# Performance work log

Measured on AMD Instinct MI355X. Metric: run time of the kernel, lower is better.

The kernel has to match this reference:

```python
import jax, jax.numpy as jnp
import numpy as np

P = 3
N_DIGITS = 4
MAX_IDX = 63  # module clamps indices with min(idx, 63)
EPS = 1e-10


def _padic_table(p=P, n_digits=N_DIGITS):
    n = p ** n_digits  # 81
    d = np.abs(np.arange(n)[:, None] - np.arange(n)[None, :])
    val = np.zeros((n, n), dtype=np.int64)
    tmp = d.copy()
    # valuation: count factors of p (at most ~n_digits*log levels; 8 iters is plenty for n=81)
    for _ in range(8):
        div = (tmp > 0) & (tmp % p == 0)
        val += div
        tmp = np.where(div, tmp // p, tmp)
    dist = np.where(d > 0, float(p) ** (-val.astype(np.float64)), 0.0)
    return jnp.asarray(dist, dtype=jnp.float32)


def setup_inputs() -> dict:
    key = jax.random.key(0)
    k1, k2 = jax.random.split(key)
    codon_embeddings = jax.random.normal(k1, (8, 1024, 256), dtype=jnp.float32)
    codon_indices = jax.random.randint(k2, (8, 1024), 0, 64)
    padic_distances = _padic_table()
    return {
        "codon_embeddings": codon_embeddings,
        "codon_indices": codon_indices,
        "padic_distances": padic_distances,
    }


def reference(codon_embeddings, codon_indices, padic_distances):
    B, S, D = codon_embeddings.shape
    x = codon_embeddings.reshape(-1, D)  # (N, D), N = B*S

    # Euclidean cdist (p=2): d2 = |xi|^2 + |xj|^2 - 2 xi.xj
    sq = jnp.sum(x * x, axis=-1)
    d2 = sq[:, None] + sq[None, :] - 2.0 * (x @ x.T)
    d2 = jnp.maximum(d2, 0.0)
    # safe sqrt (zero diag -> zero distance, no nan grads)
    emb_dist = jnp.where(d2 > 0, jnp.sqrt(jnp.where(d2 > 0, d2, 1.0)), 0.0)

    # vectorized equivalent of the python double-loop gather
    idx = jnp.minimum(codon_indices.reshape(-1), MAX_IDX)  # (N,)
    target_dist = padic_distances[idx][:, idx]  # (N, N)

    emb_n = emb_dist / (jnp.max(emb_dist) + EPS)
    tgt_n = target_dist / (jnp.max(target_dist) + EPS)

    e = emb_n.reshape(-1) - jnp.mean(emb_n)
    t = tgt_n.reshape(-1) - jnp.mean(tgt_n)
    corr = jnp.sum(e * t) / (jnp.sqrt(jnp.sum(e * e) * jnp.sum(t * t)) + EPS)
    return 1.0 - corr
```

## Files before the change

### kernel.cpp

```cpp
#include <hip/hip_runtime.h>
#include <math.h>

typedef __attribute__((ext_vector_type(8))) short short8;
typedef __attribute__((ext_vector_type(16))) float f32x16;

#if defined(__has_builtin)
#if __has_builtin(__builtin_amdgcn_global_load_lds)
#define HAVE_GLL 1
#endif
#if __has_builtin(__builtin_amdgcn_sqrtf)
#define FSQRT(x) __builtin_amdgcn_sqrtf(x)
#endif
#if __has_builtin(__builtin_amdgcn_cvt_pk_fp8_f32) && __has_builtin(__builtin_amdgcn_cvt_f32_fp8)
#define HAVE_CVT8 1
#endif
#endif
#ifndef HAVE_GLL
#define HAVE_GLL 0
#endif
#ifndef FSQRT
#define FSQRT(x) sqrtf(x)
#endif
#ifndef HAVE_CVT8
#define HAVE_CVT8 0
#endif

__device__ __forceinline__ unsigned short f2bf(float f) {
    unsigned int x = __float_as_uint(f);
    unsigned int r = (x + 0x7fffu + ((x >> 16) & 1u)) >> 16;
    return (unsigned short)r;
}

__device__ __forceinline__ unsigned char f2e4m3(float f) {
    unsigned u = __float_as_uint(f);
    unsigned s = (u >> 24) & 0x80u;
    float a = fabsf(f);
    if (a < 0.015625f) return (unsigned char)s;
    if (a > 448.f)     return (unsigned char)(s | 0x7E);
    unsigned au = u & 0x7FFFFFFFu;
    unsigned mlo = au & 0xFFFFFu;
    unsigned keep = au >> 20;
    keep += (mlo > 0x80000u) || (mlo == 0x80000u && (keep & 1u));
    int e = (int)(keep >> 3) - 127;
    unsigned m3 = keep & 7u;
    if (e < -6) return (unsigned char)s;
    if (e > 8)  return (unsigned char)(s | 0x7E);
    return (unsigned char)(s | (unsigned)((e + 7) << 3) | m3);
}
__device__ __forceinline__ float e4m3dec(unsigned char c) {
    if (!(c & 0x7F)) return 0.f;
    unsigned s = ((unsigned)(c & 0x80)) << 24;
    unsigned e = (c >> 3) & 0xF;
    unsigned m = c & 7u;
    return __uint_as_float(s | ((e - 7 + 127) << 23) | (m << 20));
}


__global__ void rowstats_kernel(const float* __restrict__ x, const int* __restrict__ idx,
                                float* __restrict__ sq, int* __restrict__ ci,
                                unsigned char* __restrict__ x8,
                                int N, int D, int doCvt) {
    int wave0 = (blockIdx.x * blockDim.x + threadIdx.x) >> 6;
    int lane  = threadIdx.x & 63;
    int nw    = (gridDim.x * blockDim.x) >> 6;
    for (int row = wave0; row < N; row += nw) {
        const float* rp = x + (size_t)row * D;
        float s = 0.f;
        for (int c = lane * 4; c < D; c += 256) {
            float4 v = *reinterpret_cast<const float4*>(rp + c);
            if (doCvt) {
#if HAVE_CVT8
                unsigned pk = 0;
                pk = (unsigned)__builtin_amdgcn_cvt_pk_fp8_f32(v.x, v.y, (int)pk, false);
                pk = (unsigned)__builtin_amdgcn_cvt_pk_fp8_f32(v.z, v.w, (int)pk, true);
                *reinterpret_cast<unsigned*>(x8 + (size_t)row * D + c) = pk;
                float q0 = __builtin_amdgcn_cvt_f32_fp8((int)pk, 0);
                float q1 = __builtin_amdgcn_cvt_f32_fp8((int)pk, 1);
                float q2 = __builtin_amdgcn_cvt_f32_fp8((int)pk, 2);
                float q3 = __builtin_amdgcn_cvt_f32_fp8((int)pk, 3);
#else
                uchar4 h;
                h.x = f2e4m3(v.x); h.y = f2e4m3(v.y); h.z = f2e4m3(v.z); h.w = f2e4m3(v.w);
                *reinterpret_cast<uchar4*>(x8 + (size_t)row * D + c) = h;
                float q0 = e4m3dec(h.x), q1 = e4m3dec(h.y), q2 = e4m3dec(h.z), q3 = e4m3dec(h.w);
#endif
                s = fmaf(q0, q0, s); s = fmaf(q1, q1, s);
                s = fmaf(q2, q2, s); s = fmaf(q3, q3, s);
            } else {
                s = fmaf(v.x, v.x, s); s = fmaf(v.y, v.y, s);
                s = fmaf(v.z, v.z, s); s = fmaf(v.w, v.w, s);
            }
        }
        #pragma unroll
        for (int o = 32; o > 0; o >>= 1) s += __shfl_down(s, o, 64);
        if (lane == 0) {
            sq[row] = s;
            int v = idx[row]; if (v > 63) v = 63;
            ci[row] = v;
        }
    }
}

__device__ __forceinline__ void tri_decode(int L, int NB, int chunks, int doSwz, int& bi, int& bj) {
    if (doSwz) { int xcd = L & 7, pos = L >> 3; L = xcd * chunks + pos; }
    float disc = (float)((2 * NB + 1) * (2 * NB + 1) - 8 * L);
    int b = (int)(((float)(2 * NB + 1) - sqrtf(disc)) * 0.5f);
    if (b < 0) b = 0; if (b > NB - 1) b = NB - 1;
    while (b + 1 <= NB - 1 && ((b + 1) * NB - ((b + 1) * b) / 2) <= L) ++b;
    while (b > 0 && (b * NB - (b * (b - 1)) / 2) > L) --b;
    bi = b; bj = b + (L - (b * NB - (b * (b - 1)) / 2));
}

template<bool DIAG>
__device__ __forceinline__ void epilogueQ(const f32x16 (&acc)[2][2],
                                          const float* sqA, const float* sqB,
                                          const int* caA, const int* cbB, const float* tbl,
                                          float* red, int w, int lane, int wr, int wc,
                                          double* partials, int pidx) {
    const int l31 = lane & 31;
    const int hi4 = (lane >> 5) << 2;
    float sb[2]; int cb[2];
    #pragma unroll
    for (int ni = 0; ni < 2; ++ni) {
        int c = wc * 64 + ni * 32 + l31;
        sb[ni] = sqB[c]; cb[ni] = cbB[c];
    }
    float se = 0.f, sd2 = 0.f, setv = 0.f;
    #pragma unroll
    for (int mi = 0; mi < 2; ++mi)
        #pragma unroll
        for (int r = 0; r < 16; ++r) {
            int rr = wr * 64 + mi * 32 + (r & 3) + ((r >> 2) << 3) + hi4;
            float sa_ = sqA[rr]; int ca_ = caA[rr];
            #pragma unroll
            for (int ni = 0; ni < 2; ++ni) {
                float d2 = fmaf(-2.f, acc[mi][ni][r], sa_ + sb[ni]);
                d2 = fmaxf(d2, 0.f);
                if (DIAG) { if (rr == wc * 64 + ni * 32 + l31) d2 = 0.f; }
                float e = FSQRT(d2);
                int delta = ca_ - cb[ni]; if (delta < 0) delta = -delta;
                float t = tbl[delta];
                se += e; sd2 += d2; setv = fmaf(e, t, setv);
            }
        }
    #pragma unroll
    for (int o = 32; o > 0; o >>= 1) {
        se  += __shfl_down(se, o, 64);
        sd2 += __shfl_down(sd2, o, 64);
        setv += __shfl_down(setv, o, 64);
    }
    if (lane == 0) { red[w * 3 + 0] = se; red[w * 3 + 1] = sd2; red[w * 3 + 2] = setv; }
    __syncthreads();
    if (w == 0 && lane == 0) {
        double wgt = DIAG ? 1.0 : 2.0;
        double S0 = 0, S1 = 0, S2 = 0;
        #pragma unroll
        for (int i = 0; i < 4; ++i) {
            S0 += (double)red[i * 3 + 0]; S1 += (double)red[i * 3 + 1]; S2 += (double)red[i * 3 + 2];
        }
        double* p = partials + (size_t)pidx * 4;
        p[0] = wgt * S0; p[1] = wgt * S1; p[2] = wgt * S2;
    }
}

__global__ __launch_bounds__(256, 4) void pair128f8_kernel(
        const unsigned char* __restrict__ x8, const float* __restrict__ table,
        const float* __restrict__ sq, const int* __restrict__ ci,
        int NB, int chunks, int doSwz, double* __restrict__ partials) {
#if HAVE_GLL
    constexpr int D = 256;
    __shared__ char lds[16384];
    __shared__ float sqA[128], sqB[128], tbl[64];
    __shared__ int   caA[128], cbB[128];
    __shared__ float red[12];

    int bi, bj;
    tri_decode(blockIdx.x, NB, chunks, doSwz, bi, bj);

    const int tid = threadIdx.x;
    const int w = tid >> 6, lane = tid & 63;
    const int wr = w >> 1, wc = w & 1;
    const int l31 = lane & 31, khalf = lane >> 5;

    if (tid < 64) tbl[tid] = table[tid];
    if (tid < 128) { sqA[tid] = sq[bi * 128 + tid]; caA[tid] = ci[bi * 128 + tid]; }
    else { int t2 = tid - 128; sqB[t2] = sq[bj * 128 + t2]; cbB[t2] = ci[bj * 128 + t2]; }

    const int pa_ = lane >> 3;
    const int pt  = ((lane & 7) - pa_) & 7;
    const int srow = pa_ * 4 + (pt >> 1);
    const int sh   = pt & 1;

    const int prow0 = ((w >= 2) ? bj : bi) * 128;
    auto STAGE4 = [&](int t) {
        #pragma unroll
        for (int q = 0; q < 4; ++q) {
            int u   = (w << 2) + q;
            int blk = (u >> 1) & 3;
            int kh  = u & 1;
            const unsigned char* g = x8 + (size_t)(prow0 + blk * 32 + srow) * D
                                        + t * 64 + kh * 32 + sh * 16;
            char* dst = lds + (u << 10);
            __builtin_amdgcn_global_load_lds(
                (__attribute__((address_space(1))) void*)(void*)g,
                (__attribute__((address_space(3))) void*)dst, 16, 0, 0);
        }
    };

    const int ra = l31 >> 2, rb = l31 & 3;
    const int pos0 = ra * 8 + ((2 * rb + 0 + ra) & 7);
    const int pos1 = ra * 8 + ((2 * rb + 1 + ra) & 7);

    f32x16 acc[2][2];
    #pragma unroll
    for (int a = 0; a < 2; ++a)
        #pragma unroll
        for (int b = 0; b < 2; ++b)
            #pragma unroll
            for (int r = 0; r < 16; ++r) acc[a][b][r] = 0.f;

    for (int t = 0; t < 4; ++t) {
        STAGE4(t);
        asm volatile("s_waitcnt vmcnt(0)" ::: "memory");
        __builtin_amdgcn_s_barrier();
        #pragma unroll
        for (int kh = 0; kh < 2; ++kh) {
            #pragma unroll
            for (int s = 0; s < 2; ++s) {
                const int fo = (s ? pos1 : pos0) * 16 + khalf * 8;
                long a_[2], b_[2];
                #pragma unroll
                for (int mi = 0; mi < 2; ++mi)
                    a_[mi] = *reinterpret_cast<const long*>(lds + (((((wr << 1) + mi) << 1) + kh) << 10) + fo);
                #pragma unroll
                for (int ni = 0; ni < 2; ++ni)
                    b_[ni] = *reinterpret_cast<const long*>(lds + ((8 + (((wc << 1) + ni) << 1) + kh) << 10) + fo);
                #pragma unroll
                for (int mi = 0; mi < 2; ++mi)
                    #pragma unroll
                    for (int ni = 0; ni < 2; ++ni)
                        acc[mi][ni] = __builtin_amdgcn_mfma_f32_32x32x16_fp8_fp8(a_[mi], b_[ni], acc[mi][ni], 0, 0, 0);
            }
        }
        __builtin_amdgcn_s_barrier();
    }

    if (bi == bj) epilogueQ<true >(acc, sqA, sqB, caA, cbB, tbl, red, w, lane, wr, wc, partials, blockIdx.x);
    else          epilogueQ<false>(acc, sqA, sqB, caA, cbB, tbl, red, w, lane, wr, wc, partials, blockIdx.x);
#endif
}

__global__ void pair_fb_kernel(const float* __restrict__ x, const float* __restrict__ table,
                               const float* __restrict__ sq, const int* __restrict__ ci,
                               int D, int NB, int chunks, int doSwz,
                               double* __restrict__ partials) {
    typedef __attribute__((ext_vector_type(4))) float f32x4v;
    int bi, bj;
    tri_decode(blockIdx.x, NB, chunks, doSwz, bi, bj);

    __shared__ float sqA[128], sqB[128], tbl[64];
    __shared__ int   caA[128], cbB[128];
    __shared__ float red[12];

    const int tid = threadIdx.x;
    const int w = tid >> 6, lane = tid & 63;
    const int wr = w >> 1, wc = w & 1;
    const int l15 = lane & 15, koct = lane >> 4;

    if (tid < 64) tbl[tid] = table[tid];
    if (tid < 128) { sqA[tid] = sq[bi * 128 + tid]; caA[tid] = ci[bi * 128 + tid]; }
    else { int t2 = tid - 128; sqB[t2] = sq[bj * 128 + t2]; cbB[t2] = ci[bj * 128 + t2]; }
    __syncthreads();

    f32x4v acc[4][4];
    #pragma unroll
    for (int a = 0; a < 4; ++a)
        #pragma unroll
        for (int b = 0; b < 4; ++b) acc[a][b] = (f32x4v){0.f, 0.f, 0.f, 0.f};

    const float* pa = x + (size_t)(bi * 128 + wr * 64 + l15) * D + koct * 8;
    const float* pb = x + (size_t)(bj * 128 + wc * 64 + l15) * D + koct * 8;
    const size_t rs = (size_t)16 * D;
    for (int k = 0; k < D; k += 32) {
        short8 af[4], bfv[4];
        #pragma unroll
        for (int m = 0; m < 4; ++m) {
            float4 f0 = *reinterpret_cast<const float4*>(pa + m * rs + k);
            float4 f1 = *reinterpret_cast<const float4*>(pa + m * rs + k + 4);
            short8 v;
            v[0]=(short)f2bf(f0.x); v[1]=(short)f2bf(f0.y); v[2]=(short)f2bf(f0.z); v[3]=(short)f2bf(f0.w);
            v[4]=(short)f2bf(f1.x); v[5]=(short)f2bf(f1.y); v[6]=(short)f2bf(f1.z); v[7]=(short)f2bf(f1.w);
            af[m] = v;
        }
        #pragma unroll
        for (int n = 0; n < 4; ++n) {
            float4 f0 = *reinterpret_cast<const float4*>(pb + n * rs + k);
            float4 f1 = *reinterpret_cast<const float4*>(pb + n * rs + k + 4);
            short8 v;
            v[0]=(short)f2bf(f0.x); v[1]=(short)f2bf(f0.y); v[2]=(short)f2bf(f0.z); v[3]=(short)f2bf(f0.w);
            v[4]=(short)f2bf(f1.x); v[5]=(short)f2bf(f1.y); v[6]=(short)f2bf(f1.z); v[7]=(short)f2bf(f1.w);
            bfv[n] = v;
        }
        #pragma unroll
        for (int fm = 0; fm < 4; ++fm)
            #pragma unroll
            for (int fn = 0; fn < 4; ++fn)
                acc[fm][fn] = __builtin_amdgcn_mfma_f32_16x16x32_bf16(af[fm], bfv[fn], acc[fm][fn], 0, 0, 0);
    }

    const int rsub = koct << 2;
    float sb[4]; int cb[4];
    #pragma unroll
    for (int fn = 0; fn < 4; ++fn) {
        int c = wc * 64 + fn * 16 + l15;
        sb[fn] = sqB[c]; cb[fn] = cbB[c];
    }
    float se = 0.f, sd2 = 0.f, setv = 0.f;
    const bool diag = (bi == bj);
    #pragma unroll
    for (int fm = 0; fm < 4; ++fm)
        #pragma unroll
        for (int rg = 0; rg < 4; ++rg) {
            int r = wr * 64 + fm * 16 + rsub + rg;
            float sa_ = sqA[r]; int ca_ = caA[r];
            #pragma unroll
            for (int fn = 0; fn < 4; ++fn) {
                float d2 = fmaf(-2.f, acc[fm][fn][rg], sa_ + sb[fn]);
                d2 = fmaxf(d2, 0.f);
                if (diag && r == wc * 64 + fn * 16 + l15) d2 = 0.f;
                float e = FSQRT(d2);
                int delta = ca_ - cb[fn]; if (delta < 0) delta = -delta;
                float t = tbl[delta];
                se += e; sd2 += d2; setv = fmaf(e, t, setv);
            }
        }
    #pragma unroll
    for (int o = 32; o > 0; o >>= 1) {
        se  += __shfl_down(se, o, 64);
        sd2 += __shfl_down(sd2, o, 64);
        setv += __shfl_down(setv, o, 64);
    }
    if (lane == 0) { red[w * 3 + 0] = se; red[w * 3 + 1] = sd2; red[w * 3 + 2] = setv; }
    __syncthreads();
    if (tid == 0) {
        double wgt = diag ? 1.0 : 2.0;
        double S0 = 0, S1 = 0, S2 = 0;
        #pragma unroll
        for (int i = 0; i < 4; ++i) {
            S0 += (double)red[i * 3 + 0]; S1 += (double)red[i * 3 + 1]; S2 += (double)red[i * 3 + 2];
        }
        double* p = partials + (size_t)blockIdx.x * 4;
        p[0] = wgt * S0; p[1] = wgt * S1; p[2] = wgt * S2;
    }
}

__global__ void finalize_kernel(const double* __restrict__ partials, int nL,
                                const int* __restrict__ civ, int N,
                                const float* __restrict__ table, int tdim,
                                float* __restrict__ out) {
    __shared__ unsigned int h[64];
    __shared__ double red[4][5];
    const int tid = threadIdx.x;
    if (tid < 64) h[tid] = 0u;
    __syncthreads();
    for (int i = tid; i < N; i += 256) atomicAdd(&h[civ[i]], 1u);
    __syncthreads();

    double se = 0, sd2 = 0, setv = 0;
    for (int i = tid; i < nL; i += 256) {
        const double* p = partials + (size_t)i * 4;
        se += p[0]; sd2 += p[1]; setv += p[2];
    }
    double st = 0, stt = 0;
    for (int c = tid; c < 4096; c += 256) {
        int u = c >> 6, v = c & 63;
        double t = (double)table[u * tdim + v];
        double hh = (double)h[u] * (double)h[v];
        st += hh * t; stt += hh * t * t;
    }
    #pragma unroll
    for (int o = 32; o > 0; o >>= 1) {
        se += __shfl_down(se, o, 64);
        sd2 += __shfl_down(sd2, o, 64);
        setv += __shfl_down(setv, o, 64);
        st += __shfl_down(st, o, 64);
        stt += __shfl_down(stt, o, 64);
    }
    int w = tid >> 6;
    if ((tid & 63) == 0) { red[w][0] = se; red[w][1] = sd2; red[w][2] = setv; red[w][3] = st; red[w][4] = stt; }
    __syncthreads();
    if (tid == 0) {
        double S[5] = {0, 0, 0, 0, 0};
        #pragma unroll
        for (int i = 0; i < 4; ++i)
            #pragma unroll
            for (int q = 0; q < 5; ++q) S[q] += red[i][q];
        double nn = (double)N * (double)N;
        double cet = S[2] - S[0] * S[3] / nn;
        double cee = S[1] - S[0] * S[0] / nn;
        double ctt = S[4] - S[3] * S[3] / nn;
        double corr = cet / (sqrt(cee * ctt) + 1e-10);
        out[0] = (float)(1.0 - corr);
    }
}

extern "C" void kernel_launch(void* const* d_in, const int* in_sizes, int n_in,
                              void* d_out, int out_size, void* d_ws, size_t ws_size,
                              hipStream_t stream) {
    const float* x     = (const float*)d_in[0];
    const int*   idx   = (const int*)d_in[1];
    const float* table = (const float*)d_in[2];

    const int N = in_sizes[1];
    const int D = in_sizes[0] / N;
    int tdim = 1;
    while (tdim * tdim < in_sizes[2]) ++tdim;

    char* ws = (char*)d_ws;
    double*        partials = (double*)(ws + 512);
    float*         sqv      = (float*)(ws + 67584);
    int*           civ      = (int*)(ws + 67584 + (size_t)N * 4);
    unsigned char* x8       = (unsigned char*)(ws + 67584 + (size_t)N * 8);

    size_t need = 67584 + (size_t)N * 8 + (size_t)N * D;
    const bool f8 = (ws_size >= need) && (D == 256) && (N % 128 == 0);

    rowstats_kernel<<<dim3(1024), 256, 0, stream>>>(x, idx, sqv, civ, x8, N, D, f8 ? 1 : 0);

    const int NB = N / 128;
    const int nL = NB * (NB + 1) / 2;
    const int doSwz = (nL % 8 == 0) ? 1 : 0;
    const int chunks = nL / 8;

    if (f8)
        pair128f8_kernel<<<dim3(nL), 256, 0, stream>>>(x8, table, sqv, civ, NB, chunks, doSwz, partials);
    else
        pair_fb_kernel<<<dim3(nL), 256, 0, stream>>>(x, table, sqv, civ, D, NB, chunks, doSwz, partials);

    finalize_kernel<<<1, 256, 0, stream>>>(partials, nL, civ, N, table, tdim, (float*)d_out);
}
```

Measured before the change: 45.47 us.

## Stage full K extent into LDS up front and drop per-step barriers

The fp8 pair kernel now issues all four K-slice global-to-LDS loads at once into a 64KB dynamic shared buffer, waits once, then runs every MFMA step with no further barriers. This removes the serialized load-wait-compute-barrier loop so memory latency is paid once per tile. In exchange LDS use per block grows to about 66KB, launch bounds drop to 2 blocks per SM, and a hipFuncSetAttribute call is added to each launch, which lowers occupancy and adds host overhead.

```diff
diff --git a/kernel.cpp b/kernel.cpp
--- a/kernel.cpp
+++ b/kernel.cpp
@@ -163,16 +163,27 @@
     }
 }
 
-__global__ __launch_bounds__(256, 4) void pair128f8_kernel(
+#define F8W_LDS_BYTES 67888
+#define F8W_TBL  65536
+#define F8W_SQA  65792
+#define F8W_SQB  66304
+#define F8W_CAA  66816
+#define F8W_CBB  67328
+#define F8W_RED  67840
+
+__global__ __launch_bounds__(256, 2) void pair128f8w_kernel(
         const unsigned char* __restrict__ x8, const float* __restrict__ table,
         const float* __restrict__ sq, const int* __restrict__ ci,
         int NB, int chunks, int doSwz, double* __restrict__ partials) {
 #if HAVE_GLL
     constexpr int D = 256;
-    __shared__ char lds[16384];
-    __shared__ float sqA[128], sqB[128], tbl[64];
-    __shared__ int   caA[128], cbB[128];
-    __shared__ float red[12];
+    extern __shared__ char dyn[];
+    float* tbl = (float*)(dyn + F8W_TBL);
+    float* sqA = (float*)(dyn + F8W_SQA);
+    float* sqB = (float*)(dyn + F8W_SQB);
+    int*   caA = (int*)(dyn + F8W_CAA);
+    int*   cbB = (int*)(dyn + F8W_CBB);
+    float* red = (float*)(dyn + F8W_RED);
 
     int bi, bj;
     tri_decode(blockIdx.x, NB, chunks, doSwz, bi, bj);
@@ -200,7 +211,7 @@
             int kh  = u & 1;
             const unsigned char* g = x8 + (size_t)(prow0 + blk * 32 + srow) * D
                                         + t * 64 + kh * 32 + sh * 16;
-            char* dst = lds + (u << 10);
+            char* dst = dyn + (((t << 4) + u) << 10);
             __builtin_amdgcn_global_load_lds(
                 (__attribute__((address_space(1))) void*)(void*)g,
                 (__attribute__((address_space(3))) void*)dst, 16, 0, 0);
@@ -219,10 +230,13 @@
             #pragma unroll
             for (int r = 0; r < 16; ++r) acc[a][b][r] = 0.f;
 
+    STAGE4(0); STAGE4(1); STAGE4(2); STAGE4(3);
+    asm volatile("s_waitcnt vmcnt(0) lgkmcnt(0)" ::: "memory");
+    __builtin_amdgcn_s_barrier();
+
+    #pragma unroll
     for (int t = 0; t < 4; ++t) {
-        STAGE4(t);
-        asm volatile("s_waitcnt vmcnt(0)" ::: "memory");
-        __builtin_amdgcn_s_barrier();
+        const int tb = t << 4;
         #pragma unroll
         for (int kh = 0; kh < 2; ++kh) {
             #pragma unroll
@@ -231,10 +245,10 @@
                 long a_[2], b_[2];
                 #pragma unroll
                 for (int mi = 0; mi < 2; ++mi)
-                    a_[mi] = *reinterpret_cast<const long*>(lds + (((((wr << 1) + mi) << 1) + kh) << 10) + fo);
+                    a_[mi] = *reinterpret_cast<const long*>(dyn + ((tb + (((wr << 1) + mi) << 1) + kh) << 10) + fo);
                 #pragma unroll
                 for (int ni = 0; ni < 2; ++ni)
-                    b_[ni] = *reinterpret_cast<const long*>(lds + ((8 + (((wc << 1) + ni) << 1) + kh) << 10) + fo);
+                    b_[ni] = *reinterpret_cast<const long*>(dyn + ((tb + 8 + (((wc << 1) + ni) << 1) + kh) << 10) + fo);
                 #pragma unroll
                 for (int mi = 0; mi < 2; ++mi)
                     #pragma unroll
@@ -242,7 +256,6 @@
                         acc[mi][ni] = __builtin_amdgcn_mfma_f32_32x32x16_fp8_fp8(a_[mi], b_[ni], acc[mi][ni], 0, 0, 0);
             }
         }
-        __builtin_amdgcn_s_barrier();
     }
 
     if (bi == bj) epilogueQ<true >(acc, sqA, sqB, caA, cbB, tbl, red, w, lane, wr, wc, partials, blockIdx.x);
@@ -423,7 +436,13 @@
     unsigned char* x8       = (unsigned char*)(ws + 67584 + (size_t)N * 8);
 
     size_t need = 67584 + (size_t)N * 8 + (size_t)N * D;
-    const bool f8 = (ws_size >= need) && (D == 256) && (N % 128 == 0);
+    bool f8 = (ws_size >= need) && (D == 256) && (N % 128 == 0);
+    if (f8) {
+        hipError_t e = hipFuncSetAttribute((const void*)pair128f8w_kernel,
+                                           hipFuncAttributeMaxDynamicSharedMemorySize,
+                                           F8W_LDS_BYTES);
+        f8 = (e == hipSuccess);
+    }
 
     rowstats_kernel<<<dim3(1024), 256, 0, stream>>>(x, idx, sqv, civ, x8, N, D, f8 ? 1 : 0);
 
@@ -433,7 +452,7 @@
     const int chunks = nL / 8;
 
     if (f8)
-        pair128f8_kernel<<<dim3(nL), 256, 0, stream>>>(x8, table, sqv, civ, NB, chunks, doSwz, partials);
+        pair128f8w_kernel<<<dim3(nL), 256, F8W_LDS_BYTES, stream>>>(x8, table, sqv, civ, NB, chunks, doSwz, partials);
     else
         pair_fb_kernel<<<dim3(nL), 256, 0, stream>>>(x, table, sqv, civ, D, NB, chunks, doSwz, partials);
 
```

Measured after the change: 53.19 us. 1.17x slower.

## Add 64x64 triangular-tile fp8 pair kernel to raise block count

Applied to the files above, without the earlier changes.

Adds a new pair kernel that processes 64x64 upper-triangular tiles with fp8 MFMA. Each of its four waves computes one 32x32 sub-tile, and operands are staged through a small 8KB LDS buffer via global_load_lds. The launcher now prefers this path, which launches 8256 blocks for N=8192 instead of 2080, to improve occupancy and load balance. The cost is more total operand reloads, more partial sums for finalize to reduce, and a per-k-step sync with no double buffering.

```diff
diff --git a/kernel.cpp b/kernel.cpp
--- a/kernel.cpp
+++ b/kernel.cpp
@@ -54,7 +54,6 @@
     unsigned m = c & 7u;
     return __uint_as_float(s | ((e - 7 + 127) << 23) | (m << 20));
 }
-
 
 __global__ void rowstats_kernel(const float* __restrict__ x, const int* __restrict__ idx,
                                 float* __restrict__ sq, int* __restrict__ ci,
@@ -111,6 +110,126 @@
     bi = b; bj = b + (L - (b * NB - (b * (b - 1)) / 2));
 }
 
+__global__ __launch_bounds__(256, 8) void pair64f8_kernel(
+        const unsigned char* __restrict__ x8, const float* __restrict__ table,
+        const float* __restrict__ sq, const int* __restrict__ ci,
+        int NB, int chunks, int doSwz, double* __restrict__ partials) {
+#if HAVE_GLL
+    constexpr int D = 256;
+    __shared__ char lds[8192];
+    __shared__ float sqA[64], sqB[64], tbl[64];
+    __shared__ int   caA[64], cbB[64];
+    __shared__ float red[12];
+
+    int bi, bj;
+    tri_decode(blockIdx.x, NB, chunks, doSwz, bi, bj);
+
+    const int tid = threadIdx.x;
+    const int w = tid >> 6, lane = tid & 63;
+    const int wr = w >> 1, wc = w & 1;
+    const int l31 = lane & 31, khalf = lane >> 5;
+
+    if (tid < 64) tbl[tid] = table[tid];
+    else if (tid < 128) { int r = tid - 64;  sqA[r] = sq[bi * 64 + r]; caA[r] = ci[bi * 64 + r]; }
+    else if (tid < 192) { int r = tid - 128; sqB[r] = sq[bj * 64 + r]; cbB[r] = ci[bj * 64 + r]; }
+
+    const int pa_ = lane >> 3;
+    const int pt  = ((lane & 7) - pa_) & 7;
+    const int srow = pa_ * 4 + (pt >> 1);
+    const int sh   = pt & 1;
+
+    const int u0 = w << 1;
+    const unsigned char* g0;
+    const unsigned char* g1;
+    {
+        int uA = u0, uB = u0 + 1;
+        int p0 = (uA < 4) ? (bi * 64 + (uA >> 1) * 32) : (bj * 64 + ((uA - 4) >> 1) * 32);
+        int p1 = (uB < 4) ? (bi * 64 + (uB >> 1) * 32) : (bj * 64 + ((uB - 4) >> 1) * 32);
+        g0 = x8 + (size_t)(p0 + srow) * D + (uA & 1) * 32 + sh * 16;
+        g1 = x8 + (size_t)(p1 + srow) * D + (uB & 1) * 32 + sh * 16;
+    }
+    char* dst0 = lds + (u0 << 10);
+    char* dst1 = lds + ((u0 + 1) << 10);
+
+    const int ra = l31 >> 2, rb = l31 & 3;
+    const int fo0 = (ra * 8 + ((2 * rb + 0 + ra) & 7)) * 16 + khalf * 8;
+    const int fo1 = (ra * 8 + ((2 * rb + 1 + ra) & 7)) * 16 + khalf * 8;
+
+    const char* a0b = lds + (((wr << 1) | 0) << 10);
+    const char* a1b = lds + (((wr << 1) | 1) << 10);
+    const char* b0b = lds + ((4 + (wc << 1) + 0) << 10);
+    const char* b1b = lds + ((4 + (wc << 1) + 1) << 10);
+
+    f32x16 acc;
+    #pragma unroll
+    for (int r = 0; r < 16; ++r) acc[r] = 0.f;
+
+    for (int t = 0; t < 4; ++t) {
+        __builtin_amdgcn_global_load_lds(
+            (__attribute__((address_space(1))) void*)(void*)g0,
+            (__attribute__((address_space(3))) void*)dst0, 16, 0, 0);
+        __builtin_amdgcn_global_load_lds(
+            (__attribute__((address_space(1))) void*)(void*)g1,
+            (__attribute__((address_space(3))) void*)dst1, 16, 0, 0);
+        g0 += 64; g1 += 64;
+        asm volatile("s_waitcnt vmcnt(0)" ::: "memory");
+        __builtin_amdgcn_s_barrier();
+        {
+            long aA, bB;
+            aA = *reinterpret_cast<const long*>(a0b + fo0);
+            bB = *reinterpret_cast<const long*>(b0b + fo0);
+            acc = __builtin_amdgcn_mfma_f32_32x32x16_fp8_fp8(aA, bB, acc, 0, 0, 0);
+            aA = *reinterpret_cast<const long*>(a0b + fo1);
+            bB = *reinterpret_cast<const long*>(b0b + fo1);
+            acc = __builtin_amdgcn_mfma_f32_32x32x16_fp8_fp8(aA, bB, acc, 0, 0, 0);
+            aA = *reinterpret_cast<const long*>(a1b + fo0);
+            bB = *reinterpret_cast<const long*>(b1b + fo0);
+            acc = __builtin_amdgcn_mfma_f32_32x32x16_fp8_fp8(aA, bB, acc, 0, 0, 0);
+            aA = *reinterpret_cast<const long*>(a1b + fo1);
+            bB = *reinterpret_cast<const long*>(b1b + fo1);
+            acc = __builtin_amdgcn_mfma_f32_32x32x16_fp8_fp8(aA, bB, acc, 0, 0, 0);
+        }
+        __builtin_amdgcn_s_barrier();
+    }
+
+    const int lcol = wc * 32 + l31;
+    const float sb = sqB[lcol];
+    const int   cb = cbB[lcol];
+    const int hi4 = khalf << 2;
+    float se = 0.f, sd2 = 0.f, setv = 0.f;
+    const bool diag = (bi == bj);
+    #pragma unroll
+    for (int r = 0; r < 16; ++r) {
+        int lrow = wr * 32 + (r & 3) + ((r >> 2) << 3) + hi4;
+        float d2 = fmaf(-2.f, acc[r], sqA[lrow] + sb);
+        d2 = fmaxf(d2, 0.f);
+        if (diag && lrow == lcol) d2 = 0.f;
+        float e = FSQRT(d2);
+        int delta = caA[lrow] - cb; if (delta < 0) delta = -delta;
+        float tt = tbl[delta];
+        se += e; sd2 += d2; setv = fmaf(e, tt, setv);
+    }
+    #pragma unroll
+    for (int o = 32; o > 0; o >>= 1) {
+        se  += __shfl_down(se, o, 64);
+        sd2 += __shfl_down(sd2, o, 64);
+        setv += __shfl_down(setv, o, 64);
+    }
+    if (lane == 0) { red[w * 3 + 0] = se; red[w * 3 + 1] = sd2; red[w * 3 + 2] = setv; }
+    __syncthreads();
+    if (tid == 0) {
+        double wgt = diag ? 1.0 : 2.0;
+        double S0 = 0, S1 = 0, S2 = 0;
+        #pragma unroll
+        for (int i = 0; i < 4; ++i) {
+            S0 += (double)red[i * 3 + 0]; S1 += (double)red[i * 3 + 1]; S2 += (double)red[i * 3 + 2];
+        }
+        double* p = partials + (size_t)blockIdx.x * 4;
+        p[0] = wgt * S0; p[1] = wgt * S1; p[2] = wgt * S2;
+    }
+#endif
+}
+
 template<bool DIAG>
 __device__ __forceinline__ void epilogueQ(const f32x16 (&acc)[2][2],
                                           const float* sqA, const float* sqB,
@@ -417,25 +536,41 @@
     while (tdim * tdim < in_sizes[2]) ++tdim;
 
     char* ws = (char*)d_ws;
-    double*        partials = (double*)(ws + 512);
-    float*         sqv      = (float*)(ws + 67584);
-    int*           civ      = (int*)(ws + 67584 + (size_t)N * 4);
-    unsigned char* x8       = (unsigned char*)(ws + 67584 + (size_t)N * 8);
-
-    size_t need = 67584 + (size_t)N * 8 + (size_t)N * D;
-    const bool f8 = (ws_size >= need) && (D == 256) && (N % 128 == 0);
-
-    rowstats_kernel<<<dim3(1024), 256, 0, stream>>>(x, idx, sqv, civ, x8, N, D, f8 ? 1 : 0);
-
-    const int NB = N / 128;
-    const int nL = NB * (NB + 1) / 2;
-    const int doSwz = (nL % 8 == 0) ? 1 : 0;
-    const int chunks = nL / 8;
-
-    if (f8)
-        pair128f8_kernel<<<dim3(nL), 256, 0, stream>>>(x8, table, sqv, civ, NB, chunks, doSwz, partials);
-    else
-        pair_fb_kernel<<<dim3(nL), 256, 0, stream>>>(x, table, sqv, civ, D, NB, chunks, doSwz, partials);
-
-    finalize_kernel<<<1, 256, 0, stream>>>(partials, nL, civ, N, table, tdim, (float*)d_out);
-}
+
+    const int NB64 = N / 64,  nL64  = NB64 * (NB64 + 1) / 2;
+    const int NB128 = N / 128, nL128 = NB128 * (NB128 + 1) / 2;
+    size_t part64_b = ((size_t)nL64 * 32 + 511) & ~(size_t)511;
+    size_t need64  = 512 + part64_b + (size_t)N * 8 + (size_t)N * D;
+    size_t need128 = 67584 + (size_t)N * 8 + (size_t)N * D;
+
+    const bool p64  = (ws_size >= need64)  && (D == 256) && (N % 64 == 0);
+    const bool p128 = !p64 && (ws_size >= need128) && (D == 256) && (N % 128 == 0);
+
+    if (p64) {
+        double*        partials = (double*)(ws + 512);
+        float*         sqv      = (float*)(ws + 512 + part64_b);
+        int*           civ      = (int*)(ws + 512 + part64_b + (size_t)N * 4);
+        unsigned char* x8       = (unsigned char*)(ws + 512 + part64_b + (size_t)N * 8);
+        rowstats_kernel<<<dim3(1024), 256, 0, stream>>>(x, idx, sqv, civ, x8, N, D, 1);
+        const int doSwz = (nL64 % 8 == 0) ? 1 : 0;
+        pair64f8_kernel<<<dim3(nL64), 256, 0, stream>>>(x8, table, sqv, civ, NB64, nL64 / 8, doSwz, partials);
+        finalize_kernel<<<1, 256, 0, stream>>>(partials, nL64, civ, N, table, tdim, (float*)d_out);
+    } else if (p128) {
+        double*        partials = (double*)(ws + 512);
+        float*         sqv      = (float*)(ws + 67584);
+        int*           civ      = (int*)(ws + 67584 + (size_t)N * 4);
+        unsigned char* x8       = (unsigned char*)(ws + 67584 + (size_t)N * 8);
+        rowstats_kernel<<<dim3(1024), 256, 0, stream>>>(x, idx, sqv, civ, x8, N, D, 1);
+        const int doSwz = (nL128 % 8 == 0) ? 1 : 0;
+        pair128f8_kernel<<<dim3(nL128), 256, 0, stream>>>(x8, table, sqv, civ, NB128, nL128 / 8, doSwz, partials);
+        finalize_kernel<<<1, 256, 0, stream>>>(partials, nL128, civ, N, table, tdim, (float*)d_out);
+    } else {
+        double* partials = (double*)(ws + 512);
+        float*  sqv      = (float*)(ws + 67584);
+        int*    civ      = (int*)(ws + 67584 + (size_t)N * 4);
+        rowstats_kernel<<<dim3(1024), 256, 0, stream>>>(x, idx, sqv, civ, (unsigned char*)0, N, D, 0);
+        const int doSwz = (nL128 % 8 == 0) ? 1 : 0;
+        pair_fb_kernel<<<dim3(nL128), 256, 0, stream>>>(x, table, sqv, civ, D, NB128, nL128 / 8, doSwz, partials);
+        finalize_kernel<<<1, 256, 0, stream>>>(partials, nL128, civ, N, table, tdim, (float*)d_out);
+    }
+}
```

Measured after the change: 59.46 us. 30.8% more time.

## Split each 128x128 pair tile across sixteen waves with one MFMA tile each

Applied to the files above, without the earlier changes.

The fp8 pair kernel now launches 1024 threads per block. Each of the 16 waves owns a single 32x32 accumulator tile instead of a 2x2 grid of tiles, and each wave stages exactly one 1KB LDS chunk per k-step. The epilogue is inlined and reduces across 16 waves. The aim is more waves in flight to hide LDS/global latency and shorten the per-wave MFMA and epilogue chain. The cost is that A/B fragments are no longer reused across tiles inside a wave, so LDS reads per MFMA double. The larger block also adds barrier cost and may reduce the number of resident blocks per CU.

```diff
diff --git a/kernel.cpp b/kernel.cpp
--- a/kernel.cpp
+++ b/kernel.cpp
@@ -54,7 +54,6 @@
     unsigned m = c & 7u;
     return __uint_as_float(s | ((e - 7 + 127) << 23) | (m << 20));
 }
-
 
 __global__ void rowstats_kernel(const float* __restrict__ x, const int* __restrict__ idx,
                                 float* __restrict__ sq, int* __restrict__ ci,
@@ -111,59 +110,7 @@
     bi = b; bj = b + (L - (b * NB - (b * (b - 1)) / 2));
 }
 
-template<bool DIAG>
-__device__ __forceinline__ void epilogueQ(const f32x16 (&acc)[2][2],
-                                          const float* sqA, const float* sqB,
-                                          const int* caA, const int* cbB, const float* tbl,
-                                          float* red, int w, int lane, int wr, int wc,
-                                          double* partials, int pidx) {
-    const int l31 = lane & 31;
-    const int hi4 = (lane >> 5) << 2;
-    float sb[2]; int cb[2];
-    #pragma unroll
-    for (int ni = 0; ni < 2; ++ni) {
-        int c = wc * 64 + ni * 32 + l31;
-        sb[ni] = sqB[c]; cb[ni] = cbB[c];
-    }
-    float se = 0.f, sd2 = 0.f, setv = 0.f;
-    #pragma unroll
-    for (int mi = 0; mi < 2; ++mi)
-        #pragma unroll
-        for (int r = 0; r < 16; ++r) {
-            int rr = wr * 64 + mi * 32 + (r & 3) + ((r >> 2) << 3) + hi4;
-            float sa_ = sqA[rr]; int ca_ = caA[rr];
-            #pragma unroll
-            for (int ni = 0; ni < 2; ++ni) {
-                float d2 = fmaf(-2.f, acc[mi][ni][r], sa_ + sb[ni]);
-                d2 = fmaxf(d2, 0.f);
-                if (DIAG) { if (rr == wc * 64 + ni * 32 + l31) d2 = 0.f; }
-                float e = FSQRT(d2);
-                int delta = ca_ - cb[ni]; if (delta < 0) delta = -delta;
-                float t = tbl[delta];
-                se += e; sd2 += d2; setv = fmaf(e, t, setv);
-            }
-        }
-    #pragma unroll
-    for (int o = 32; o > 0; o >>= 1) {
-        se  += __shfl_down(se, o, 64);
-        sd2 += __shfl_down(sd2, o, 64);
-        setv += __shfl_down(setv, o, 64);
-    }
-    if (lane == 0) { red[w * 3 + 0] = se; red[w * 3 + 1] = sd2; red[w * 3 + 2] = setv; }
-    __syncthreads();
-    if (w == 0 && lane == 0) {
-        double wgt = DIAG ? 1.0 : 2.0;
-        double S0 = 0, S1 = 0, S2 = 0;
-        #pragma unroll
-        for (int i = 0; i < 4; ++i) {
-            S0 += (double)red[i * 3 + 0]; S1 += (double)red[i * 3 + 1]; S2 += (double)red[i * 3 + 2];
-        }
-        double* p = partials + (size_t)pidx * 4;
-        p[0] = wgt * S0; p[1] = wgt * S1; p[2] = wgt * S2;
-    }
-}
-
-__global__ __launch_bounds__(256, 4) void pair128f8_kernel(
+__global__ __launch_bounds__(1024, 2) void pair128w16_kernel(
         const unsigned char* __restrict__ x8, const float* __restrict__ table,
         const float* __restrict__ sq, const int* __restrict__ ci,
         int NB, int chunks, int doSwz, double* __restrict__ partials) {
@@ -172,81 +119,110 @@
     __shared__ char lds[16384];
     __shared__ float sqA[128], sqB[128], tbl[64];
     __shared__ int   caA[128], cbB[128];
-    __shared__ float red[12];
+    __shared__ float red[48];
 
     int bi, bj;
     tri_decode(blockIdx.x, NB, chunks, doSwz, bi, bj);
 
     const int tid = threadIdx.x;
     const int w = tid >> 6, lane = tid & 63;
-    const int wr = w >> 1, wc = w & 1;
+    const int qr = w >> 2, qc = w & 3;
     const int l31 = lane & 31, khalf = lane >> 5;
 
-    if (tid < 64) tbl[tid] = table[tid];
     if (tid < 128) { sqA[tid] = sq[bi * 128 + tid]; caA[tid] = ci[bi * 128 + tid]; }
-    else { int t2 = tid - 128; sqB[t2] = sq[bj * 128 + t2]; cbB[t2] = ci[bj * 128 + t2]; }
+    else if (tid < 256) { int r = tid - 128; sqB[r] = sq[bj * 128 + r]; cbB[r] = ci[bj * 128 + r]; }
+    else if (tid < 320) { int r = tid - 256; tbl[r] = table[r]; }
 
     const int pa_ = lane >> 3;
     const int pt  = ((lane & 7) - pa_) & 7;
     const int srow = pa_ * 4 + (pt >> 1);
     const int sh   = pt & 1;
 
-    const int prow0 = ((w >= 2) ? bj : bi) * 128;
-    auto STAGE4 = [&](int t) {
-        #pragma unroll
-        for (int q = 0; q < 4; ++q) {
-            int u   = (w << 2) + q;
-            int blk = (u >> 1) & 3;
-            int kh  = u & 1;
-            const unsigned char* g = x8 + (size_t)(prow0 + blk * 32 + srow) * D
-                                        + t * 64 + kh * 32 + sh * 16;
-            char* dst = lds + (u << 10);
-            __builtin_amdgcn_global_load_lds(
-                (__attribute__((address_space(1))) void*)(void*)g,
-                (__attribute__((address_space(3))) void*)dst, 16, 0, 0);
-        }
-    };
+    const int isB  = (w >= 8);
+    const int blk  = (isB ? (w - 8) : w) >> 1;
+    const int kh_w = w & 1;
+    const unsigned char* gsrc = x8 + (size_t)((isB ? bj : bi) * 128 + blk * 32 + srow) * D
+                                   + kh_w * 32 + sh * 16;
+    char* dst = lds + (w << 10);
 
     const int ra = l31 >> 2, rb = l31 & 3;
-    const int pos0 = ra * 8 + ((2 * rb + 0 + ra) & 7);
-    const int pos1 = ra * 8 + ((2 * rb + 1 + ra) & 7);
-
-    f32x16 acc[2][2];
-    #pragma unroll
-    for (int a = 0; a < 2; ++a)
-        #pragma unroll
-        for (int b = 0; b < 2; ++b)
-            #pragma unroll
-            for (int r = 0; r < 16; ++r) acc[a][b][r] = 0.f;
-
-    for (int t = 0; t < 4; ++t) {
-        STAGE4(t);
+    const int fo0 = (ra * 8 + ((2 * rb + 0 + ra) & 7)) * 16 + khalf * 8;
+    const int fo1 = (ra * 8 + ((2 * rb + 1 + ra) & 7)) * 16 + khalf * 8;
+
+    const char* aU0 = lds + (((qr << 1) | 0) << 10);
+    const char* aU1 = lds + (((qr << 1) | 1) << 10);
+    const char* bU0 = lds + ((8 + ((qc << 1) | 0)) << 10);
+    const char* bU1 = lds + ((8 + ((qc << 1) | 1)) << 10);
+
+    f32x16 acc;
+    #pragma unroll
+    for (int r = 0; r < 16; ++r) acc[r] = 0.f;
+
+    #define STAGE1(t) \
+        __builtin_amdgcn_global_load_lds( \
+            (__attribute__((address_space(1))) void*)(void*)(gsrc + (t) * 64), \
+            (__attribute__((address_space(3))) void*)dst, 16, 0, 0)
+    #define COMPUTE() { \
+        long a_, b_; \
+        a_ = *reinterpret_cast<const long*>(aU0 + fo0); b_ = *reinterpret_cast<const long*>(bU0 + fo0); \
+        acc = __builtin_amdgcn_mfma_f32_32x32x16_fp8_fp8(a_, b_, acc, 0, 0, 0); \
+        a_ = *reinterpret_cast<const long*>(aU0 + fo1); b_ = *reinterpret_cast<const long*>(bU0 + fo1); \
+        acc = __builtin_amdgcn_mfma_f32_32x32x16_fp8_fp8(a_, b_, acc, 0, 0, 0); \
+        a_ = *reinterpret_cast<const long*>(aU1 + fo0); b_ = *reinterpret_cast<const long*>(bU1 + fo0); \
+        acc = __builtin_amdgcn_mfma_f32_32x32x16_fp8_fp8(a_, b_, acc, 0, 0, 0); \
+        a_ = *reinterpret_cast<const long*>(aU1 + fo1); b_ = *reinterpret_cast<const long*>(bU1 + fo1); \
+        acc = __builtin_amdgcn_mfma_f32_32x32x16_fp8_fp8(a_, b_, acc, 0, 0, 0); \
+    }
+
+    STAGE1(0);
+    __syncthreads();
+    COMPUTE();
+    #pragma unroll
+    for (int t = 1; t < 4; ++t) {
+        __builtin_amdgcn_s_barrier();
+        STAGE1(t);
         asm volatile("s_waitcnt vmcnt(0)" ::: "memory");
         __builtin_amdgcn_s_barrier();
-        #pragma unroll
-        for (int kh = 0; kh < 2; ++kh) {
-            #pragma unroll
-            for (int s = 0; s < 2; ++s) {
-                const int fo = (s ? pos1 : pos0) * 16 + khalf * 8;
-                long a_[2], b_[2];
-                #pragma unroll
-                for (int mi = 0; mi < 2; ++mi)
-                    a_[mi] = *reinterpret_cast<const long*>(lds + (((((wr << 1) + mi) << 1) + kh) << 10) + fo);
-                #pragma unroll
-                for (int ni = 0; ni < 2; ++ni)
-                    b_[ni] = *reinterpret_cast<const long*>(lds + ((8 + (((wc << 1) + ni) << 1) + kh) << 10) + fo);
-                #pragma unroll
-                for (int mi = 0; mi < 2; ++mi)
-                    #pragma unroll
-                    for (int ni = 0; ni < 2; ++ni)
-                        acc[mi][ni] = __builtin_amdgcn_mfma_f32_32x32x16_fp8_fp8(a_[mi], b_[ni], acc[mi][ni], 0, 0, 0);
-            }
-        }
-        __builtin_amdgcn_s_barrier();
-    }
-
-    if (bi == bj) epilogueQ<true >(acc, sqA, sqB, caA, cbB, tbl, red, w, lane, wr, wc, partials, blockIdx.x);
-    else          epilogueQ<false>(acc, sqA, sqB, caA, cbB, tbl, red, w, lane, wr, wc, partials, blockIdx.x);
+        COMPUTE();
+    }
+    #undef STAGE1
+    #undef COMPUTE
+
+    const int lcol = qc * 32 + l31;
+    const float sb = sqB[lcol];
+    const int   cb = cbB[lcol];
+    const int hi4 = khalf << 2;
+    float se = 0.f, sd2 = 0.f, setv = 0.f;
+    const bool diag = (bi == bj);
+    #pragma unroll
+    for (int r = 0; r < 16; ++r) {
+        int lrow = qr * 32 + (r & 3) + ((r >> 2) << 3) + hi4;
+        float d2 = fmaf(-2.f, acc[r], sqA[lrow] + sb);
+        d2 = fmaxf(d2, 0.f);
+        if (diag && lrow == lcol) d2 = 0.f;
+        float e = FSQRT(d2);
+        int delta = caA[lrow] - cb; if (delta < 0) delta = -delta;
+        float tt = tbl[delta];
+        se += e; sd2 += d2; setv = fmaf(e, tt, setv);
+    }
+    #pragma unroll
+    for (int o = 32; o > 0; o >>= 1) {
+        se  += __shfl_down(se, o, 64);
+        sd2 += __shfl_down(sd2, o, 64);
+        setv += __shfl_down(setv, o, 64);
+    }
+    if (lane == 0) { red[w * 3 + 0] = se; red[w * 3 + 1] = sd2; red[w * 3 + 2] = setv; }
+    __syncthreads();
+    if (tid == 0) {
+        double wgt = diag ? 1.0 : 2.0;
+        double S0 = 0, S1 = 0, S2 = 0;
+        #pragma unroll
+        for (int i = 0; i < 16; ++i) {
+            S0 += (double)red[i * 3 + 0]; S1 += (double)red[i * 3 + 1]; S2 += (double)red[i * 3 + 2];
+        }
+        double* p = partials + (size_t)blockIdx.x * 4;
+        p[0] = wgt * S0; p[1] = wgt * S1; p[2] = wgt * S2;
+    }
 #endif
 }
 
@@ -433,7 +409,7 @@
     const int chunks = nL / 8;
 
     if (f8)
-        pair128f8_kernel<<<dim3(nL), 256, 0, stream>>>(x8, table, sqv, civ, NB, chunks, doSwz, partials);
+        pair128w16_kernel<<<dim3(nL), 1024, 0, stream>>>(x8, table, sqv, civ, NB, chunks, doSwz, partials);
     else
         pair_fb_kernel<<<dim3(nL), 256, 0, stream>>>(x, table, sqv, civ, D, NB, chunks, doSwz, partials);
 
```

Result: slower. 59.14 us (+30.1%).
